# Kernel optimization log

Measured on AMD Instinct MI355X. Metric: run time of the kernel, lower is better.

The kernel has to match this reference:

```python
import jax, jax.numpy as jnp
import numpy as np

L = 100  # hidden size of lstm1 (module hardcodes self.L = 100)


def _lstm_cell(x, h, c, W_ih, W_hh, b_ih, b_hh):
    # PyTorch LSTMCell: gates ordered (input, forget, cell, output)
    gates = x @ W_ih.T + h @ W_hh.T + b_ih + b_hh  # [B, 4*H]
    i, f, g, o = jnp.split(gates, 4, axis=-1)
    i = jax.nn.sigmoid(i)
    f = jax.nn.sigmoid(f)
    g = jnp.tanh(g)
    o = jax.nn.sigmoid(o)
    c_new = f * c + i * g
    h_new = o * jnp.tanh(c_new)
    return h_new, c_new


def setup_inputs() -> dict:
    key = jax.random.key(0)
    ks = jax.random.split(key, 9)
    B, T = 4096, 2048
    s1 = 1.0 / np.sqrt(L)   # torch LSTMCell init scale for hidden 100
    s2 = 1.0                # hidden size 1 -> scale 1
    return {
        "input": jax.random.normal(ks[0], (B, T), dtype=jnp.float32),
        "W_ih1": jax.random.uniform(ks[1], (4 * L, 1), jnp.float32, -s1, s1),
        "W_hh1": jax.random.uniform(ks[2], (4 * L, L), jnp.float32, -s1, s1),
        "b_ih1": jax.random.uniform(ks[3], (4 * L,), jnp.float32, -s1, s1),
        "b_hh1": jax.random.uniform(ks[4], (4 * L,), jnp.float32, -s1, s1),
        "W_ih2": jax.random.uniform(ks[5], (4, L), jnp.float32, -s2, s2),
        "W_hh2": jax.random.uniform(ks[6], (4, 1), jnp.float32, -s2, s2),
        "b_ih2": jax.random.uniform(ks[7], (4,), jnp.float32, -s2, s2),
        "b_hh2": jax.random.uniform(ks[8], (4,), jnp.float32, -s2, s2),
    }


def reference(input, W_ih1, W_hh1, b_ih1, b_hh1, W_ih2, W_hh2, b_ih2, b_hh2):
    B, T = input.shape
    x_seq = input.T[:, :, None]  # [T, B, 1]
    h1 = jnp.zeros((B, L), input.dtype)
    c1 = jnp.zeros((B, L), input.dtype)
    h2 = jnp.zeros((B, 1), input.dtype)
    c2 = jnp.zeros((B, 1), input.dtype)

    def step(carry, x_t):
        h1, c1, h2, c2 = carry
        h1, c1 = _lstm_cell(x_t, h1, c1, W_ih1, W_hh1, b_ih1, b_hh1)
        h2, c2 = _lstm_cell(h1, h2, c2, W_ih2, W_hh2, b_ih2, b_hh2)
        return (h1, c1, h2, c2), h2  # emit h2: [B, 1]

    _, outs = jax.lax.scan(step, (h1, c1, h2, c2), x_seq)
    # outs: [T, B, 1] -> stack along time dim then squeeze, matching torch.stack(.,1).squeeze(2)
    return outs[:, :, 0].T  # [B, T]
```

## Files before the change

### kernel.cpp

```cpp
#include <hip/hip_runtime.h>
#include <math.h>

#define BB 4096
#define TT 2048
#define LL 100

constexpr int NB = 16;
constexpr int WG = 448;

#define L2E 1.44269504088896340736f

#define AH(kt, row) (((kt) * 64 + ((row) ^ ((row) >> 3))) * 4)

typedef short bf16x8 __attribute__((ext_vector_type(8)));
typedef float f32x4 __attribute__((ext_vector_type(4)));

union AF { int4 v; bf16x8 f; unsigned int w[4]; };

__device__ __forceinline__ float frcp(float x) { return __builtin_amdgcn_rcpf(x); }
__device__ __forceinline__ float fexp2(float x) {
#if __has_builtin(__builtin_amdgcn_exp2f)
    return __builtin_amdgcn_exp2f(x);
#else
    return exp2f(x);
#endif
}
__device__ __forceinline__ float sig2(float xp) { return frcp(1.0f + fexp2(-xp)); }
__device__ __forceinline__ float th2(float xpp) { return 1.0f - 2.0f * frcp(1.0f + fexp2(xpp)); }
__device__ __forceinline__ float ftanh_n(float x) { return th2(2.0f * L2E * x); }

__device__ __forceinline__ unsigned int xor1_lane(unsigned int v) {
#if __has_builtin(__builtin_amdgcn_mov_dpp)
    return (unsigned int)__builtin_amdgcn_mov_dpp((int)v, 0xB1, 0xF, 0xF, false);
#else
    return (unsigned int)__shfl_xor((int)v, 1, 64);
#endif
}
__device__ __forceinline__ unsigned int cvt_pk_bf16(float lo, float hi) {
    unsigned int d;
    asm("v_cvt_pk_bf16_f32 %0, %1, %2" : "=v"(d) : "v"(lo), "v"(hi));
    return d;
}

__global__ void __launch_bounds__(WG)
__attribute__((amdgpu_waves_per_eu(2, 2)))
lstm2_kernel(const float* __restrict__ input,
             const float* __restrict__ W_ih1,
             const float* __restrict__ W_hh1,
             const float* __restrict__ b_ih1,
             const float* __restrict__ b_hh1,
             const float* __restrict__ W_ih2,
             const float* __restrict__ W_hh2,
             const float* __restrict__ b_ih2,
             const float* __restrict__ b_hh2,
             float* __restrict__ out)
{
    __shared__ __align__(16) unsigned int afragH[2][1024];
    __shared__ __align__(16) unsigned int afragL[2][1024];

    const int tid = threadIdx.x;
    const int wave = tid >> 6;
    const int lane = tid & 63;
    const int col16 = lane & 15;
    const int quad = lane >> 4;
    const int bg0 = blockIdx.x * NB;

    for (int i = tid; i < 2 * 1024; i += WG) {
        (&afragH[0][0])[i] = 0u;
        (&afragL[0][0])[i] = 0u;
    }

    const int sb = (wave == 3) ? 6 : ((wave < 3) ? wave : wave - 1);
    const int uu = 16 * sb + col16;
    const bool uvalid = (uu < LL);
    const bool l2lane = (wave == 3) && (col16 == 8);
    const bool xlane = (wave == 3) && (col16 == 4);

    const float gsc[4] = {L2E, L2E, 2.0f * L2E, L2E};

    bf16x8 bhi[4][4], bmid[4][4];
#pragma unroll
    for (int g = 0; g < 4; ++g)
#pragma unroll
        for (int kt = 0; kt < 4; ++kt)
#pragma unroll
            for (int j = 0; j < 8; ++j) {
                const int k = 32 * kt + 8 * quad + j;
                float w = 0.0f;
                if (k < LL) {
                    if (l2lane)       w = W_ih2[g * LL + k] * gsc[g];
                    else if (uvalid)  w = W_hh1[(100 * g + uu) * LL + k] * gsc[g];
                } else if (k == 100) {
                    if (!l2lane && uvalid) w = W_ih1[100 * g + uu] * gsc[g];
                }
                const unsigned int hh = cvt_pk_bf16(w, 0.0f) & 0xffffu;
                bhi[g][kt][j] = (short)hh;
                const float wres = w - __uint_as_float(hh << 16);
                bmid[g][kt][j] = (short)(cvt_pk_bf16(wres, 0.0f) & 0xffffu);
            }

    f32x4 binit[4];
#pragma unroll
    for (int g = 0; g < 4; ++g) {
        float bv = 0.0f;
        if (l2lane)      bv = (b_ih2[g] + b_hh2[g]) * gsc[g];
        else if (uvalid) bv = (b_ih1[100 * g + uu] + b_hh1[100 * g + uu]) * gsc[g];
        binit[g] = (f32x4){bv, bv, bv, bv};
    }

    float c1[4] = {0.f, 0.f, 0.f, 0.f};

    const int kt_u = uu >> 5;
    const int lnb = ((uu >> 3) & 3) * 16;
    const int jh = (uu & 7) >> 1;
    const bool oddu = (uu & 1) != 0;

    float wh2s[4], h2v[4] = {0.f, 0.f, 0.f, 0.f}, c2v[4] = {0.f, 0.f, 0.f, 0.f};
#pragma unroll
    for (int g = 0; g < 4; ++g)
        wh2s[g] = l2lane ? W_hh2[g] * gsc[g] : 0.0f;

    __syncthreads();

    if (wave == 3 && (col16 == 4 || col16 == 5)) {
#pragma unroll
        for (int r = 0; r < 4; ++r) {
            const int m = 4 * quad + r;
            const float h = (col16 == 4) ? input[(size_t)(bg0 + m) * TT] : 0.0f;
            const float hq = __uint_as_float(xor1_lane(__float_as_uint(h)));
            const unsigned int tpk = cvt_pk_bf16(h, hq);
            const float hl_own = h - __uint_as_float(tpk << 16);
            const float hl_par = hq - __uint_as_float(tpk & 0xffff0000u);
            const unsigned int lod = cvt_pk_bf16(hl_par, hl_own);
            (oddu ? afragL[0] : afragH[0])[AH(kt_u, lnb + m) + jh] = oddu ? lod : tpk;
        }
    }
    __syncthreads();

    for (int t = 0; t <= TT; ++t) {
        const int p = t & 1, pn = p ^ 1;

        if (t < TT || wave == 3) {
            float xnext[4] = {0.f, 0.f, 0.f, 0.f};
            if (xlane && t + 1 < TT) {
#pragma unroll
                for (int r = 0; r < 4; ++r)
                    xnext[r] = input[(size_t)(bg0 + 4 * quad + r) * TT + (t + 1)];
            }

            AF ahi[4];
#pragma unroll
            for (int kt = 0; kt < 4; ++kt)
                ahi[kt].v = *(const int4*)&afragH[p][AH(kt, lane)];

            f32x4 acc[4];
#pragma unroll
            for (int g = 0; g < 4; ++g)
                acc[g] = __builtin_amdgcn_mfma_f32_16x16x32_bf16(ahi[0].f, bhi[g][0], binit[g], 0, 0, 0);
#pragma unroll
            for (int kt = 1; kt < 4; ++kt)
#pragma unroll
                for (int g = 0; g < 4; ++g)
                    acc[g] = __builtin_amdgcn_mfma_f32_16x16x32_bf16(ahi[kt].f, bhi[g][kt], acc[g], 0, 0, 0);
#pragma unroll
            for (int kt = 0; kt < 4; ++kt)
#pragma unroll
                for (int g = 0; g < 4; ++g)
                    acc[g] = __builtin_amdgcn_mfma_f32_16x16x32_bf16(ahi[kt].f, bmid[g][kt], acc[g], 0, 0, 0);

            AF alo[4];
#pragma unroll
            for (int kt = 0; kt < 4; ++kt)
                alo[kt].v = *(const int4*)&afragL[p][AH(kt, lane)];
#pragma unroll
            for (int kt = 0; kt < 4; ++kt)
#pragma unroll
                for (int g = 0; g < 4; ++g)
                    acc[g] = __builtin_amdgcn_mfma_f32_16x16x32_bf16(alo[kt].f, bhi[g][kt], acc[g], 0, 0, 0);

            if (l2lane && t >= 1) {
#pragma unroll
                for (int r = 0; r < 4; ++r) {
                    const float p0 = fmaf(wh2s[0], h2v[r], acc[0][r]);
                    const float p1 = fmaf(wh2s[1], h2v[r], acc[1][r]);
                    const float p2 = fmaf(wh2s[2], h2v[r], acc[2][r]);
                    const float p3 = fmaf(wh2s[3], h2v[r], acc[3][r]);
                    const float i2 = sig2(p0), f2 = sig2(p1), g2 = th2(p2), o2 = sig2(p3);
                    c2v[r] = f2 * c2v[r] + i2 * g2;
                    h2v[r] = o2 * ftanh_n(c2v[r]);
                    out[(size_t)(bg0 + 4 * quad + r) * TT + (t - 1)] = h2v[r];
                }
            }

            if (t < TT) {
                unsigned int* const wpl = oddu ? afragL[pn] : afragH[pn];
#pragma unroll
                for (int r = 0; r < 4; ++r) {
                    const int m = 4 * quad + r;
                    const float iv = sig2(acc[0][r]);
                    const float fv = sig2(acc[1][r]);
                    const float gv = th2(acc[2][r]);
                    const float ov = sig2(acc[3][r]);
                    const float c = fv * c1[r] + iv * gv;
                    c1[r] = c;
                    const float h = uvalid ? (ov * ftanh_n(c)) : xnext[r];
                    const float hq = __uint_as_float(xor1_lane(__float_as_uint(h)));
                    const unsigned int tpk = cvt_pk_bf16(h, hq);
                    const float hl_own = h - __uint_as_float(tpk << 16);
                    const float hl_par = hq - __uint_as_float(tpk & 0xffff0000u);
                    const unsigned int lod = cvt_pk_bf16(hl_par, hl_own);
                    wpl[AH(kt_u, lnb + m) + jh] = oddu ? lod : tpk;
                }
            }
        }

        __syncthreads();
    }
}

extern "C" void kernel_launch(void* const* d_in, const int* in_sizes, int n_in,
                              void* d_out, int out_size, void* d_ws, size_t ws_size,
                              hipStream_t stream) {
    const float* input = (const float*)d_in[0];
    const float* W_ih1 = (const float*)d_in[1];
    const float* W_hh1 = (const float*)d_in[2];
    const float* b_ih1 = (const float*)d_in[3];
    const float* b_hh1 = (const float*)d_in[4];
    const float* W_ih2 = (const float*)d_in[5];
    const float* W_hh2 = (const float*)d_in[6];
    const float* b_ih2 = (const float*)d_in[7];
    const float* b_hh2 = (const float*)d_in[8];
    float* out = (float*)d_out;

    dim3 grid(BB / NB);
    dim3 block(WG);
    lstm2_kernel<<<grid, block, 0, stream>>>(input, W_ih1, W_hh1, b_ih1, b_hh1,
                                             W_ih2, W_hh2, b_ih2, b_hh2, out);
}
```

Measured before the change: 2.739 ms.

## Interleave last MFMA per gate with activations, prefetch low fragments, skip dead writes

Loads the low-part A fragments up front alongside the high fragments. The last low-part MFMA for each gate is split out, so the sigmoid and tanh work for the input, forget and cell gates overlaps the remaining MFMAs. The low-fragment buffer gets a separate XOR swizzle (AL) to spread LDS bank accesses, and lanes whose unit index is past the used range no longer write to LDS. The cell-state update now runs before the output gate's MFMA finishes. The cost is higher register pressure and extra scheduling dependencies.

```diff
diff --git a/kernel.cpp b/kernel.cpp
--- a/kernel.cpp
+++ b/kernel.cpp
@@ -11,6 +11,7 @@
 #define L2E 1.44269504088896340736f
 
 #define AH(kt, row) (((kt) * 64 + ((row) ^ ((row) >> 3))) * 4)
+#define AL(kt, row) (((kt) * 64 + (((row) ^ ((row) >> 3)) ^ 1)) * 4)
 
 typedef short bf16x8 __attribute__((ext_vector_type(8)));
 typedef float f32x4 __attribute__((ext_vector_type(4)));
@@ -75,6 +76,7 @@
     const bool uvalid = (uu < LL);
     const bool l2lane = (wave == 3) && (col16 == 8);
     const bool xlane = (wave == 3) && (col16 == 4);
+    const bool wr_en = (uu <= 101);
 
     const float gsc[4] = {L2E, L2E, 2.0f * L2E, L2E};
 
@@ -132,7 +134,8 @@
             const float hl_own = h - __uint_as_float(tpk << 16);
             const float hl_par = hq - __uint_as_float(tpk & 0xffff0000u);
             const unsigned int lod = cvt_pk_bf16(hl_par, hl_own);
-            (oddu ? afragL[0] : afragH[0])[AH(kt_u, lnb + m) + jh] = oddu ? lod : tpk;
+            if (oddu) afragL[0][AL(3, lnb + m) + jh] = lod;
+            else      afragH[0][AH(3, lnb + m) + jh] = tpk;
         }
     }
     __syncthreads();
@@ -148,10 +151,13 @@
                     xnext[r] = input[(size_t)(bg0 + 4 * quad + r) * TT + (t + 1)];
             }
 
-            AF ahi[4];
+            AF ahi[4], alo[4];
 #pragma unroll
             for (int kt = 0; kt < 4; ++kt)
                 ahi[kt].v = *(const int4*)&afragH[p][AH(kt, lane)];
+#pragma unroll
+            for (int kt = 0; kt < 4; ++kt)
+                alo[kt].v = *(const int4*)&afragL[p][AL(kt, lane)];
 
             f32x4 acc[4];
 #pragma unroll
@@ -167,16 +173,32 @@
 #pragma unroll
                 for (int g = 0; g < 4; ++g)
                     acc[g] = __builtin_amdgcn_mfma_f32_16x16x32_bf16(ahi[kt].f, bmid[g][kt], acc[g], 0, 0, 0);
-
-            AF alo[4];
-#pragma unroll
-            for (int kt = 0; kt < 4; ++kt)
-                alo[kt].v = *(const int4*)&afragL[p][AH(kt, lane)];
-#pragma unroll
-            for (int kt = 0; kt < 4; ++kt)
+#pragma unroll
+            for (int kt = 0; kt < 3; ++kt)
 #pragma unroll
                 for (int g = 0; g < 4; ++g)
                     acc[g] = __builtin_amdgcn_mfma_f32_16x16x32_bf16(alo[kt].f, bhi[g][kt], acc[g], 0, 0, 0);
+
+            float iv[4], fv[4], ta[4];
+
+            acc[0] = __builtin_amdgcn_mfma_f32_16x16x32_bf16(alo[3].f, bhi[0][3], acc[0], 0, 0, 0);
+#pragma unroll
+            for (int r = 0; r < 4; ++r) iv[r] = sig2(acc[0][r]);
+
+            acc[1] = __builtin_amdgcn_mfma_f32_16x16x32_bf16(alo[3].f, bhi[1][3], acc[1], 0, 0, 0);
+#pragma unroll
+            for (int r = 0; r < 4; ++r) fv[r] = sig2(acc[1][r]);
+
+            acc[2] = __builtin_amdgcn_mfma_f32_16x16x32_bf16(alo[3].f, bhi[2][3], acc[2], 0, 0, 0);
+#pragma unroll
+            for (int r = 0; r < 4; ++r) {
+                const float gv = th2(acc[2][r]);
+                const float c = fv[r] * c1[r] + iv[r] * gv;
+                c1[r] = c;
+                ta[r] = 2.0f * L2E * c;
+            }
+
+            acc[3] = __builtin_amdgcn_mfma_f32_16x16x32_bf16(alo[3].f, bhi[3][3], acc[3], 0, 0, 0);
 
             if (l2lane && t >= 1) {
 #pragma unroll
@@ -193,23 +215,21 @@
             }
 
             if (t < TT) {
-                unsigned int* const wpl = oddu ? afragL[pn] : afragH[pn];
 #pragma unroll
                 for (int r = 0; r < 4; ++r) {
                     const int m = 4 * quad + r;
-                    const float iv = sig2(acc[0][r]);
-                    const float fv = sig2(acc[1][r]);
-                    const float gv = th2(acc[2][r]);
                     const float ov = sig2(acc[3][r]);
-                    const float c = fv * c1[r] + iv * gv;
-                    c1[r] = c;
-                    const float h = uvalid ? (ov * ftanh_n(c)) : xnext[r];
+                    const float th = th2(ta[r]);
+                    const float h = uvalid ? (ov * th) : xnext[r];
                     const float hq = __uint_as_float(xor1_lane(__float_as_uint(h)));
                     const unsigned int tpk = cvt_pk_bf16(h, hq);
                     const float hl_own = h - __uint_as_float(tpk << 16);
                     const float hl_par = hq - __uint_as_float(tpk & 0xffff0000u);
                     const unsigned int lod = cvt_pk_bf16(hl_par, hl_own);
-                    wpl[AH(kt_u, lnb + m) + jh] = oddu ? lod : tpk;
+                    if (wr_en) {
+                        if (oddu) afragL[pn][AL(kt_u, lnb + m) + jh] = lod;
+                        else      afragH[pn][AH(kt_u, lnb + m) + jh] = tpk;
+                    }
                 }
             }
         }
```

New measurement: 3.010 ms. 1.1x slower.
